# Optimization experiments

Hardware: AMD Instinct MI355X
Metric: run time of the kernel (lower is better)

The kernel has to match this reference:

```python
import jax, jax.numpy as jnp
import numpy as np

N = 1048576
NUM_POINTS = 9
L = 3
EPS = 1e-6
GMM_EPS = 1e-6  # diagonal regularizer used by the GaussianMixture fit


def _det2(m):
    return m[..., 0, 0] * m[..., 1, 1] - m[..., 0, 1] * m[..., 1, 0]


def _inv2(m, det):
    # closed-form 2x2 inverse via adjugate
    adj = jnp.stack([
        jnp.stack([m[..., 1, 1], -m[..., 0, 1]], axis=-1),
        jnp.stack([-m[..., 1, 0], m[..., 0, 0]], axis=-1),
    ], axis=-2)
    return adj / det[..., None, None]


def setup_inputs() -> dict:
    key = jax.random.key(0)
    k1, k2, k3, k4, k5, k6 = jax.random.split(key, 6)
    # ground-truth rotated rectangles -> 4 corners (N, 4, 2)
    center = jax.random.uniform(k1, (N, 2), jnp.float32, 0.0, 512.0)
    w = jax.random.uniform(k2, (N,), jnp.float32, 10.0, 60.0)
    h = jax.random.uniform(k3, (N,), jnp.float32, 10.0, 60.0)
    th = jax.random.uniform(k4, (N,), jnp.float32, 0.0, np.pi)
    c, s = jnp.cos(th), jnp.sin(th)
    # local corners ordered so edge 0->1 is the width axis, 1->2 the height axis
    lx = jnp.stack([-w, w, w, -w], axis=1) * 0.5  # (N,4)
    ly = jnp.stack([-h, -h, h, h], axis=1) * 0.5
    gx = c[:, None] * lx - s[:, None] * ly + center[:, 0:1]
    gy = s[:, None] * lx + c[:, None] * ly + center[:, 1:2]
    target = jnp.stack([gx, gy], axis=-1).astype(jnp.float32)  # (N,4,2)
    # predicted convex points scattered around the box center
    pred = center[:, None, :] + 5.0 * jax.random.normal(k5, (N, NUM_POINTS, 2), jnp.float32)
    return {"pred": pred, "target": target}


def reference(pred, target):
    pred = pred.reshape(-1, NUM_POINTS, 2)
    target = target.reshape(-1, 4, 2)
    # --- GMM fit (1 component) == closed-form MLE Gaussian ---
    p_mu = pred.mean(axis=1)                       # (N,2)
    xm = pred - p_mu[:, None, :]                   # (N,9,2)
    p_var = jnp.einsum('nki,nkj->nij', xm, xm) / NUM_POINTS \
        + GMM_EPS * jnp.eye(2, dtype=pred.dtype)   # (N,2,2)
    # --- gt2gaussian ---
    t_mu = target.mean(axis=1)                     # (N,2)
    e1 = target[:, 1, :] - target[:, 0, :]
    e2 = target[:, 2, :] - target[:, 1, :]
    w = jnp.sum(e1 * e1, axis=-1)                  # (N,)
    h = jnp.sum(e2 * e2, axis=-1)
    cs = e1 / jnp.sqrt(w)[:, None]                 # (cos, sin)
    c, s = cs[:, 0], cs[:, 1]
    R = jnp.stack([jnp.stack([c, -s], axis=-1),
                   jnp.stack([s, c], axis=-1)], axis=-2)  # (N,2,2)
    d = jnp.stack([w, h], axis=-1) / (4.0 * L * L)         # (N,2)
    t_var = jnp.einsum('nij,nj,nkj->nik', R, d, R)         # (N,2,2)
    # --- KLD(pred || target) with closed-form 2x2 inverse/det ---
    t_det = _det2(t_var)
    p_det = _det2(p_var)
    t_inv = _inv2(t_var, t_det)
    delta = p_mu - t_mu                            # (N,2)
    term1 = jnp.einsum('ni,nij,nj->n', delta, t_inv, delta)
    trace = jnp.einsum('nij,nji->n', t_inv, p_var)
    term2 = trace + jnp.log(t_det / p_det)
    kld = 0.5 * (term1 + term2) - 1.0
    kl_agg = jnp.maximum(kld, EPS)
    loss = 1.0 - 1.0 / (2.0 + jnp.sqrt(kl_agg))    # (N,)
    return loss.mean()  # loss_weight = 1.0, reduction = 'mean'
```

## Files before the change

### kernel.cpp

```cpp
#include <hip/hip_runtime.h>


__device__ __forceinline__ float kld_elem(
    const float px[9], const float py[9],
    const float tx[4], const float ty[4])
{
    const float inv9 = 1.0f / 9.0f;
    float sx = 0.f, sy = 0.f;
    #pragma unroll
    for (int k = 0; k < 9; ++k) { sx += px[k]; sy += py[k]; }
    float mux = sx * inv9, muy = sy * inv9;
    float a = 0.f, b = 0.f, d = 0.f;
    #pragma unroll
    for (int k = 0; k < 9; ++k) {
        float xx = px[k] - mux, yy = py[k] - muy;
        a += xx * xx; b += xx * yy; d += yy * yy;
    }
    a = a * inv9 + 1e-6f;
    b = b * inv9;
    d = d * inv9 + 1e-6f;

    float tmux = (tx[0] + tx[1] + tx[2] + tx[3]) * 0.25f;
    float tmuy = (ty[0] + ty[1] + ty[2] + ty[3]) * 0.25f;
    float e1x = tx[1] - tx[0], e1y = ty[1] - ty[0];
    float e2x = tx[2] - tx[1], e2y = ty[2] - ty[1];
    float w = e1x * e1x + e1y * e1y;
    float h = e2x * e2x + e2y * e2y;
    float sw = sqrtf(w);
    float c = e1x / sw, s = e1y / sw;
    const float invLL = 1.0f / 36.0f;
    float dw = w * invLL, dh = h * invLL;
    float tv00 = c * c * dw + s * s * dh;
    float tv01 = c * s * (dw - dh);
    float tv11 = s * s * dw + c * c * dh;

    float t_det = tv00 * tv11 - tv01 * tv01;
    float p_det = a * d - b * b;
    float inv_tdet = 1.0f / t_det;

    float dx = mux - tmux, dy = muy - tmuy;
    float term1 = (dx * dx * tv11 - 2.0f * dx * dy * tv01 + dy * dy * tv00) * inv_tdet;
    float trace = (tv11 * a - 2.0f * tv01 * b + tv00 * d) * inv_tdet;
    float term2 = trace + logf(t_det / p_det);
    float kld = 0.5f * (term1 + term2) - 1.0f;
    float kl = fmaxf(kld, 1e-6f);
    return 1.0f - 1.0f / (2.0f + sqrtf(kl));
}

#define ELEMS_PER_THREAD 4

__global__ __launch_bounds__(256) void kld_partial_kernel(
    const float* __restrict__ pred,
    const float* __restrict__ target,
    float* __restrict__ ws,
    int n_total)
{
    const int idx0   = blockIdx.x * 256 + threadIdx.x;
    const int stride = gridDim.x * 256;

    float loss = 0.0f;

    #pragma unroll
    for (int i = 0; i < ELEMS_PER_THREAD; ++i) {
        int e = idx0 + i * stride;
        if (e < n_total) {
            const float2* p = reinterpret_cast<const float2*>(pred) + (size_t)e * 9;
            const float2* t = reinterpret_cast<const float2*>(target) + (size_t)e * 4;
            float2 p0 = p[0], p1 = p[1], p2 = p[2], p3 = p[3], p4 = p[4],
                   p5 = p[5], p6 = p[6], p7 = p[7], p8 = p[8];
            float2 q0 = t[0], q1 = t[1], q2 = t[2], q3 = t[3];

            float px[9] = {p0.x, p1.x, p2.x, p3.x, p4.x, p5.x, p6.x, p7.x, p8.x};
            float py[9] = {p0.y, p1.y, p2.y, p3.y, p4.y, p5.y, p6.y, p7.y, p8.y};
            float tx[4] = {q0.x, q1.x, q2.x, q3.x};
            float ty[4] = {q0.y, q1.y, q2.y, q3.y};
            loss += kld_elem(px, py, tx, ty);
        }
    }

    #pragma unroll
    for (int off = 32; off > 0; off >>= 1)
        loss += __shfl_down(loss, off, 64);

    __shared__ float sm[4];
    int lane = threadIdx.x & 63;
    int wid  = threadIdx.x >> 6;
    if (lane == 0) sm[wid] = loss;
    __syncthreads();
    if (threadIdx.x == 0)
        ws[blockIdx.x] = sm[0] + sm[1] + sm[2] + sm[3];
}

__global__ __launch_bounds__(256) void kld_final_kernel(
    const float* __restrict__ ws, float* __restrict__ out,
    int nblocks, float inv_n)
{
    float s = 0.0f;
    for (int i = threadIdx.x; i < nblocks; i += 256)
        s += ws[i];

    #pragma unroll
    for (int off = 32; off > 0; off >>= 1)
        s += __shfl_down(s, off, 64);

    __shared__ float sm[4];
    int lane = threadIdx.x & 63;
    int wid  = threadIdx.x >> 6;
    if (lane == 0) sm[wid] = s;
    __syncthreads();
    if (threadIdx.x == 0)
        out[0] = (sm[0] + sm[1] + sm[2] + sm[3]) * inv_n;
}

extern "C" void kernel_launch(void* const* d_in, const int* in_sizes, int n_in,
                              void* d_out, int out_size, void* d_ws, size_t ws_size,
                              hipStream_t stream) {
    const float* pred   = (const float*)d_in[0];
    const float* target = (const float*)d_in[1];
    float* out = (float*)d_out;
    float* ws  = (float*)d_ws;

    int n = in_sizes[0] / 18;
    int nblocks = (n + 256 * ELEMS_PER_THREAD - 1) / (256 * ELEMS_PER_THREAD);
    if (nblocks < 1) nblocks = 1;

    kld_partial_kernel<<<nblocks, 256, 0, stream>>>(pred, target, ws, n);
    kld_final_kernel<<<1, 256, 0, stream>>>(ws, out, nblocks, 1.0f / (float)n);
}
```

Measured before the change: 134.7 us.

## Stage per-wave chunks into LDS via global_load_lds with double buffering

Each wave now owns chunks of 64 elements and copies the pred and target bytes into LDS using coalesced direct global-to-LDS loads, so no element is read with strided per-thread float2 accesses. The next chunk is prefetched into a second buffer while the current one is computed, with manual vmcnt/lgkmcnt waits. Threads then read their elements from LDS and handle the tail separately. This adds LDS traffic, uses about 53KB of LDS per block, which may limit occupancy, and relies on hand-written waitcnt values being correct.

```diff
diff --git a/kernel.cpp b/kernel.cpp
--- a/kernel.cpp
+++ b/kernel.cpp
@@ -1,5 +1,7 @@
 #include <hip/hip_runtime.h>
 
+
+#define WAVES_PER_BLOCK 4
 
 __device__ __forceinline__ float kld_elem(
     const float px[9], const float py[9],
@@ -47,7 +49,42 @@
     return 1.0f - 1.0f / (2.0f + sqrtf(kl));
 }
 
-#define ELEMS_PER_THREAD 4
+__device__ __forceinline__ float kld_direct(
+    const float* __restrict__ pred, const float* __restrict__ target, size_t e)
+{
+    const float2* p = reinterpret_cast<const float2*>(pred) + e * 9;
+    const float2* t = reinterpret_cast<const float2*>(target) + e * 4;
+    float2 p0 = p[0], p1 = p[1], p2 = p[2], p3 = p[3], p4 = p[4],
+           p5 = p[5], p6 = p[6], p7 = p[7], p8 = p[8];
+    float2 q0 = t[0], q1 = t[1], q2 = t[2], q3 = t[3];
+    float px[9] = {p0.x, p1.x, p2.x, p3.x, p4.x, p5.x, p6.x, p7.x, p8.x};
+    float py[9] = {p0.y, p1.y, p2.y, p3.y, p4.y, p5.y, p6.y, p7.y, p8.y};
+    float tx[4] = {q0.x, q1.x, q2.x, q3.x};
+    float ty[4] = {q0.y, q1.y, q2.y, q3.y};
+    return kld_elem(px, py, tx, ty);
+}
+
+__device__ __forceinline__ void gload_lds4(const float* g, float* l)
+{
+    __builtin_amdgcn_global_load_lds(
+        (const __attribute__((address_space(1))) void*)g,
+        (__attribute__((address_space(3))) void*)l,
+        4, 0, 0);
+}
+
+__device__ __forceinline__ void stage_chunk(
+    const float* __restrict__ pred, const float* __restrict__ target,
+    float* ldsreg, size_t chunk, int lane)
+{
+    const float* pg = pred   + chunk * 1152 + lane;
+    const float* tg = target + chunk * 512  + lane;
+    #pragma unroll
+    for (int k = 0; k < 18; ++k)
+        gload_lds4(pg + k * 64, ldsreg + k * 64);
+    #pragma unroll
+    for (int k = 0; k < 8; ++k)
+        gload_lds4(tg + k * 64, ldsreg + 1152 + k * 64);
+}
 
 __global__ __launch_bounds__(256) void kld_partial_kernel(
     const float* __restrict__ pred,
@@ -55,36 +92,62 @@
     float* __restrict__ ws,
     int n_total)
 {
-    const int idx0   = blockIdx.x * 256 + threadIdx.x;
-    const int stride = gridDim.x * 256;
+    __shared__ __align__(16) float lds[WAVES_PER_BLOCK][2][1664];
+
+    const int lane        = threadIdx.x & 63;
+    const int wid         = threadIdx.x >> 6;
+    const int wave_gid    = blockIdx.x * WAVES_PER_BLOCK + wid;
+    const int total_waves = gridDim.x * WAVES_PER_BLOCK;
+    const int full_chunks = n_total >> 6;
 
     float loss = 0.0f;
 
-    #pragma unroll
-    for (int i = 0; i < ELEMS_PER_THREAD; ++i) {
-        int e = idx0 + i * stride;
-        if (e < n_total) {
-            const float2* p = reinterpret_cast<const float2*>(pred) + (size_t)e * 9;
-            const float2* t = reinterpret_cast<const float2*>(target) + (size_t)e * 4;
-            float2 p0 = p[0], p1 = p[1], p2 = p[2], p3 = p[3], p4 = p[4],
-                   p5 = p[5], p6 = p[6], p7 = p[7], p8 = p[8];
-            float2 q0 = t[0], q1 = t[1], q2 = t[2], q3 = t[3];
+    const int tail = n_total & 63;
+    if (wave_gid == 0 && lane < tail)
+        loss += kld_direct(pred, target, (size_t)full_chunks * 64 + lane);
 
-            float px[9] = {p0.x, p1.x, p2.x, p3.x, p4.x, p5.x, p6.x, p7.x, p8.x};
-            float py[9] = {p0.y, p1.y, p2.y, p3.y, p4.y, p5.y, p6.y, p7.y, p8.y};
-            float tx[4] = {q0.x, q1.x, q2.x, q3.x};
-            float ty[4] = {q0.y, q1.y, q2.y, q3.y};
-            loss += kld_elem(px, py, tx, ty);
+    float* lds0 = &lds[wid][0][0];
+    float* lds1 = &lds[wid][1][0];
+
+    int c = wave_gid;
+    if (c < full_chunks)
+        stage_chunk(pred, target, lds0, (size_t)c, lane);
+
+    int cur = 0;
+    for (; c < full_chunks; c += total_waves) {
+        float* ldscur = cur ? lds1 : lds0;
+        float* ldsnxt = cur ? lds0 : lds1;
+
+        asm volatile("s_waitcnt lgkmcnt(0)" ::: "memory");
+
+        const int nxt = c + total_waves;
+        if (nxt < full_chunks) {
+            stage_chunk(pred, target, ldsnxt, (size_t)nxt, lane);
+            asm volatile("s_waitcnt vmcnt(26)" ::: "memory");
+        } else {
+            asm volatile("s_waitcnt vmcnt(0)" ::: "memory");
         }
+
+        const float2* pe = reinterpret_cast<const float2*>(ldscur) + lane * 9;
+        float2 p0 = pe[0], p1 = pe[1], p2 = pe[2], p3 = pe[3], p4 = pe[4],
+               p5 = pe[5], p6 = pe[6], p7 = pe[7], p8 = pe[8];
+        const float4* te = reinterpret_cast<const float4*>(ldscur + 1152) + lane * 2;
+        float4 t01 = te[0], t23 = te[1];
+
+        float px[9] = {p0.x, p1.x, p2.x, p3.x, p4.x, p5.x, p6.x, p7.x, p8.x};
+        float py[9] = {p0.y, p1.y, p2.y, p3.y, p4.y, p5.y, p6.y, p7.y, p8.y};
+        float tx[4] = {t01.x, t01.z, t23.x, t23.z};
+        float ty[4] = {t01.y, t01.w, t23.y, t23.w};
+        loss += kld_elem(px, py, tx, ty);
+
+        cur ^= 1;
     }
 
     #pragma unroll
     for (int off = 32; off > 0; off >>= 1)
         loss += __shfl_down(loss, off, 64);
 
-    __shared__ float sm[4];
-    int lane = threadIdx.x & 63;
-    int wid  = threadIdx.x >> 6;
+    __shared__ float sm[WAVES_PER_BLOCK];
     if (lane == 0) sm[wid] = loss;
     __syncthreads();
     if (threadIdx.x == 0)
@@ -121,7 +184,7 @@
     float* ws  = (float*)d_ws;
 
     int n = in_sizes[0] / 18;
-    int nblocks = (n + 256 * ELEMS_PER_THREAD - 1) / (256 * ELEMS_PER_THREAD);
+    int nblocks = (n + 256 * 4 - 1) / (256 * 4);
     if (nblocks < 1) nblocks = 1;
 
     kld_partial_kernel<<<nblocks, 256, 0, stream>>>(pred, target, ws, n);
```

Measured after the change: 135.6 us. No clear change (+0.7%).

## Fuse final reduction via last-block atomic counter, nontemporal vector loads, EPT 2

Applied to the files above, without the earlier changes.

Merges the two-kernel reduction into a single kernel in which the last block to finish, detected with an atomic counter and threadfence, sums the per-block partials. Loads switch to nontemporal builtins, with the target read as two float4 instead of four float2, and elements per thread drop from 4 to 2 so more blocks are launched. A hipMemsetAsync is added to reset the counter, which replaces the second kernel launch with a memset on the stream. The launch-overhead saving may be small relative to a bandwidth-bound main pass.

```diff
diff --git a/kernel.cpp b/kernel.cpp
--- a/kernel.cpp
+++ b/kernel.cpp
@@ -1,5 +1,10 @@
 #include <hip/hip_runtime.h>
 
+
+typedef float v2f __attribute__((ext_vector_type(2)));
+typedef float v4f __attribute__((ext_vector_type(4)));
+
+#define EPT 2
 
 __device__ __forceinline__ float kld_elem(
     const float px[9], const float py[9],
@@ -47,33 +52,41 @@
     return 1.0f - 1.0f / (2.0f + sqrtf(kl));
 }
 
-#define ELEMS_PER_THREAD 4
-
-__global__ __launch_bounds__(256) void kld_partial_kernel(
+__global__ __launch_bounds__(256) void kld_fused_kernel(
     const float* __restrict__ pred,
     const float* __restrict__ target,
+    float* __restrict__ out,
     float* __restrict__ ws,
-    int n_total)
+    int n_total, float inv_n)
 {
-    const int idx0   = blockIdx.x * 256 + threadIdx.x;
+    const int tid    = threadIdx.x;
+    const int idx0   = blockIdx.x * 256 + tid;
     const int stride = gridDim.x * 256;
 
     float loss = 0.0f;
 
     #pragma unroll
-    for (int i = 0; i < ELEMS_PER_THREAD; ++i) {
+    for (int i = 0; i < EPT; ++i) {
         int e = idx0 + i * stride;
         if (e < n_total) {
-            const float2* p = reinterpret_cast<const float2*>(pred) + (size_t)e * 9;
-            const float2* t = reinterpret_cast<const float2*>(target) + (size_t)e * 4;
-            float2 p0 = p[0], p1 = p[1], p2 = p[2], p3 = p[3], p4 = p[4],
-                   p5 = p[5], p6 = p[6], p7 = p[7], p8 = p[8];
-            float2 q0 = t[0], q1 = t[1], q2 = t[2], q3 = t[3];
+            const v2f* p = reinterpret_cast<const v2f*>(pred) + (size_t)e * 9;
+            const v4f* t = reinterpret_cast<const v4f*>(target) + (size_t)e * 2;
+            v2f p0 = __builtin_nontemporal_load(p + 0);
+            v2f p1 = __builtin_nontemporal_load(p + 1);
+            v2f p2 = __builtin_nontemporal_load(p + 2);
+            v2f p3 = __builtin_nontemporal_load(p + 3);
+            v2f p4 = __builtin_nontemporal_load(p + 4);
+            v2f p5 = __builtin_nontemporal_load(p + 5);
+            v2f p6 = __builtin_nontemporal_load(p + 6);
+            v2f p7 = __builtin_nontemporal_load(p + 7);
+            v2f p8 = __builtin_nontemporal_load(p + 8);
+            v4f t01 = __builtin_nontemporal_load(t + 0);
+            v4f t23 = __builtin_nontemporal_load(t + 1);
 
             float px[9] = {p0.x, p1.x, p2.x, p3.x, p4.x, p5.x, p6.x, p7.x, p8.x};
             float py[9] = {p0.y, p1.y, p2.y, p3.y, p4.y, p5.y, p6.y, p7.y, p8.y};
-            float tx[4] = {q0.x, q1.x, q2.x, q3.x};
-            float ty[4] = {q0.y, q1.y, q2.y, q3.y};
+            float tx[4] = {t01.x, t01.z, t23.x, t23.z};
+            float ty[4] = {t01.y, t01.w, t23.y, t23.w};
             loss += kld_elem(px, py, tx, ty);
         }
     }
@@ -83,33 +96,37 @@
         loss += __shfl_down(loss, off, 64);
 
     __shared__ float sm[4];
-    int lane = threadIdx.x & 63;
-    int wid  = threadIdx.x >> 6;
+    __shared__ int amLast;
+    const int lane = tid & 63;
+    const int wid  = tid >> 6;
     if (lane == 0) sm[wid] = loss;
     __syncthreads();
-    if (threadIdx.x == 0)
-        ws[blockIdx.x] = sm[0] + sm[1] + sm[2] + sm[3];
-}
 
-__global__ __launch_bounds__(256) void kld_final_kernel(
-    const float* __restrict__ ws, float* __restrict__ out,
-    int nblocks, float inv_n)
-{
-    float s = 0.0f;
-    for (int i = threadIdx.x; i < nblocks; i += 256)
-        s += ws[i];
+    if (tid == 0) {
+        float bsum = sm[0] + sm[1] + sm[2] + sm[3];
+        ws[1 + blockIdx.x] = bsum;
+        __threadfence();
+        unsigned prev = atomicAdd(reinterpret_cast<unsigned*>(ws), 1u);
+        amLast = (prev == gridDim.x - 1);
+    }
+    __syncthreads();
 
-    #pragma unroll
-    for (int off = 32; off > 0; off >>= 1)
-        s += __shfl_down(s, off, 64);
+    if (amLast) {
+        __threadfence();
+        float s = 0.0f;
+        const int nb = (int)gridDim.x;
+        for (int i = tid; i < nb; i += 256)
+            s += ws[1 + i];
 
-    __shared__ float sm[4];
-    int lane = threadIdx.x & 63;
-    int wid  = threadIdx.x >> 6;
-    if (lane == 0) sm[wid] = s;
-    __syncthreads();
-    if (threadIdx.x == 0)
-        out[0] = (sm[0] + sm[1] + sm[2] + sm[3]) * inv_n;
+        #pragma unroll
+        for (int off = 32; off > 0; off >>= 1)
+            s += __shfl_down(s, off, 64);
+
+        if (lane == 0) sm[wid] = s;
+        __syncthreads();
+        if (tid == 0)
+            out[0] = (sm[0] + sm[1] + sm[2] + sm[3]) * inv_n;
+    }
 }
 
 extern "C" void kernel_launch(void* const* d_in, const int* in_sizes, int n_in,
@@ -121,9 +138,11 @@
     float* ws  = (float*)d_ws;
 
     int n = in_sizes[0] / 18;
-    int nblocks = (n + 256 * ELEMS_PER_THREAD - 1) / (256 * ELEMS_PER_THREAD);
+    int nblocks = (n + 256 * EPT - 1) / (256 * EPT);
     if (nblocks < 1) nblocks = 1;
 
-    kld_partial_kernel<<<nblocks, 256, 0, stream>>>(pred, target, ws, n);
-    kld_final_kernel<<<1, 256, 0, stream>>>(ws, out, nblocks, 1.0f / (float)n);
+    hipMemsetAsync(d_ws, 0, 4, stream);
+
+    kld_fused_kernel<<<nblocks, 256, 0, stream>>>(
+        pred, target, out, ws, n, 1.0f / (float)n);
 }
```

Measured after the change: 241.6 us. 79.4% more time.
